# Performance work log

Hardware: AMD Instinct MI355X
Metric: run time of the kernel (lower is better)

## Reference

```python
import jax, jax.numpy as jnp
import numpy as np

# DCNv2 config (matches init_kwargs)
STRIDE, PAD, DIL = 1, 1, 1
KH, KW = 3, 3
K = KH * KW


def setup_inputs() -> dict:
    key = jax.random.key(0)
    k1, k2, k3, k4 = jax.random.split(key, 4)
    B, C, H, W = 2, 256, 96, 96
    O = 256
    inp = jax.random.normal(k1, (B, C, H, W), jnp.float32)
    # offset channels interleaved (dy, dx) per kernel tap -> 2*K channels
    offset = jax.random.normal(k2, (B, 2 * K, H, W), jnp.float32)
    # modulation mask in [0,1) (sigmoid is applied outside this module in DCN heads)
    mask = jax.random.uniform(k3, (B, K, H, W), jnp.float32)
    n = C * KH * KW
    stdv = 1.0 / float(np.sqrt(n))
    weight = jax.random.uniform(k4, (O, C, KH, KW), jnp.float32, -stdv, stdv)
    bias = jnp.zeros((O,), jnp.float32)
    return {"input": inp, "offset": offset, "mask": mask, "weight": weight, "bias": bias}


def reference(input, offset, mask, weight, bias):
    B, C, H, W = input.shape
    O = weight.shape[0]
    Ho = (H + 2 * PAD - DIL * (KH - 1) - 1) // STRIDE + 1
    Wo = (W + 2 * PAD - DIL * (KW - 1) - 1) // STRIDE + 1

    # learned per-pixel offsets: channel layout [dy_k0, dx_k0, dy_k1, dx_k1, ...]
    dy = offset[:, 0::2]  # [B,K,Ho,Wo]
    dx = offset[:, 1::2]  # [B,K,Ho,Wo]

    ky = (jnp.arange(K) // KW * DIL).astype(jnp.float32)  # kernel tap row offsets
    kx = (jnp.arange(K) % KW * DIL).astype(jnp.float32)   # kernel tap col offsets
    base_y = (jnp.arange(Ho) * STRIDE - PAD).astype(jnp.float32)
    base_x = (jnp.arange(Wo) * STRIDE - PAD).astype(jnp.float32)

    # sampling positions, [B,K,Ho,Wo]
    y = base_y[None, None, :, None] + ky[None, :, None, None] + dy
    x = base_x[None, None, None, :] + kx[None, :, None, None] + dx

    y0 = jnp.floor(y)
    x0 = jnp.floor(x)
    wy = y - y0  # bilinear fractional weights
    wx = x - x0

    inp_flat = input.reshape(B, C, H * W)

    def gather(yi, xi):
        # zero-padded bilinear corner gather: out-of-bounds -> 0
        ii = yi.astype(jnp.int32)
        jj = xi.astype(jnp.int32)
        valid = ((ii >= 0) & (ii < H) & (jj >= 0) & (jj < W)).astype(input.dtype)
        idx = jnp.clip(ii, 0, H - 1) * W + jnp.clip(jj, 0, W - 1)  # [B,K,Ho,Wo]
        v = jnp.take_along_axis(inp_flat, idx.reshape(B, 1, -1), axis=2)  # [B,C,K*Ho*Wo]
        return v * valid.reshape(B, 1, -1)

    v00 = gather(y0, x0)
    v01 = gather(y0, x0 + 1)
    v10 = gather(y0 + 1, x0)
    v11 = gather(y0 + 1, x0 + 1)

    wyf = wy.reshape(B, 1, -1)
    wxf = wx.reshape(B, 1, -1)
    sampled = (v00 * (1 - wyf) * (1 - wxf) + v01 * (1 - wyf) * wxf
               + v10 * wyf * (1 - wxf) + v11 * wyf * wxf)  # [B,C,K*Ho*Wo]

    mod = sampled * mask.reshape(B, 1, -1)           # modulation per tap/pixel
    mod = mod.reshape(B, C, K, Ho * Wo)
    out = jnp.einsum('bcks,ock->bos', mod, weight.reshape(O, C, K)) + bias[None, :, None]
    return out.reshape(B, O, Ho, Wo)
```

## Files before the change

### kernel.cpp

```cpp
#include <hip/hip_runtime.h>
#include <hip/hip_bf16.h>


#define Hh 96
#define Ww 96
#define Cc 256
#define Oo 256
#define Bb 2
#define Kk 9
#define Ss (Hh * Ww)
#define CKTOT (Cc * Kk)

typedef __bf16 bf16x8 __attribute__((ext_vector_type(8)));
typedef __bf16 bf16x2v __attribute__((ext_vector_type(2)));
typedef float f32x16 __attribute__((ext_vector_type(16)));
typedef float f32x2 __attribute__((ext_vector_type(2)));

__device__ __forceinline__ f32x2 up2(unsigned u) {
  f32x2 r;
  r.x = __uint_as_float(u << 16);
  r.y = __uint_as_float(u & 0xffff0000u);
  return r;
}

__device__ __forceinline__ void barrier_lgkm() {
  asm volatile("" ::: "memory");
  __builtin_amdgcn_s_waitcnt(0xC07F);
  __builtin_amdgcn_s_barrier();
  asm volatile("" ::: "memory");
}

__global__ __launch_bounds__(256) void prep(const float* __restrict__ inp,
                                            const float* __restrict__ wsrc,
                                            __bf16* __restrict__ it,
                                            __bf16* __restrict__ wt) {
  __shared__ float tile[64][65];
  const int bx = blockIdx.x;
  const int tid = threadIdx.x;

  if (bx < 1152) {
    const int hw0 = (bx % 144) * 64;
    const int c0 = ((bx / 144) & 3) * 64;
    const int b = bx / 576;
    const int hw_l = tid & 63, cr = tid >> 6;
    const float* src = inp + ((size_t)(b * Cc + c0) * Ss) + hw0;
#pragma unroll
    for (int r = 0; r < 16; ++r) {
      int c_l = r * 4 + cr;
      tile[c_l][hw_l] = src[(size_t)c_l * Ss + hw_l];
    }
    __syncthreads();
    const int cp = (tid & 31) * 2, hr = tid >> 5;
    __bf16* dst = it + ((size_t)(b * Ss + hw0) * Cc) + c0;
#pragma unroll
    for (int r = 0; r < 8; ++r) {
      int hw_s = r * 8 + hr;
      bf16x2v p;
      p.x = (__bf16)tile[cp][hw_s];
      p.y = (__bf16)tile[cp + 1][hw_s];
      *(bf16x2v*)(dst + (size_t)hw_s * Cc + cp) = p;
    }
  } else {
    int i = (bx - 1152) * 256 + tid;
    int j = i & 7;
    int l = (i >> 3) & 63;
    int cc = (i >> 9) & 15;
    int osub = (i >> 13) & 7;
    int kk = i >> 16;
    int o = osub * 32 + (l & 31);
    int ch = cc * 16 + ((l >> 5) << 3) + j;
    wt[i] = (__bf16)wsrc[(o * Cc + ch) * Kk + kk];
  }
}

__global__ __launch_bounds__(256, 4) void dcn_main(
    const __bf16* __restrict__ it,
    const __bf16* __restrict__ wt,
    const float* __restrict__ offset,
    const float* __restrict__ mask,
    const float* __restrict__ bias,
    float* __restrict__ out)
{
  __shared__ __bf16 colB[32 * 32 * 8];
  __shared__ int4 pa9[9][32];
  __shared__ float4 pw9[9][32];

  const int tid = threadIdx.x;
  const int tile = (blockIdx.x & 7) * 36 + (blockIdx.x >> 3);
  const int s0 = tile * 32;
  const int b = blockIdx.y;
  const int lane = tid & 63;
  const int wv = tid >> 6;
  const int sB = lane & 31;
  const int hi = lane >> 5;
  const int fs = tid & 31;
  const int gb = ((tid >> 5) & 1) + ((tid >> 6) << 1);

  const char* itb = (const char*)(it + (size_t)b * Ss * Cc);

  for (int idx = tid; idx < 9 * 32; idx += 256) {
    int kk = idx >> 5;
    int sl = idx & 31;
    int s = s0 + sl;
    int ho = s / Ww;
    int wo = s - ho * Ww;
    float dy = offset[((size_t)(b * 18 + 2 * kk)) * Ss + s];
    float dx = offset[((size_t)(b * 18 + 2 * kk + 1)) * Ss + s];
    float m = mask[((size_t)(b * 9 + kk)) * Ss + s];
    float y = (float)(ho - 1 + kk / 3) + dy;
    float x = (float)(wo - 1 + kk % 3) + dx;
    float fy = floorf(y), fx = floorf(x);
    int y0 = (int)fy, x0 = (int)fx;
    float wy = y - fy, wx = x - fx;
    int y1 = y0 + 1, x1 = x0 + 1;
    float vy0 = (y0 >= 0 && y0 < Hh) ? 1.f : 0.f;
    float vy1 = (y1 >= 0 && y1 < Hh) ? 1.f : 0.f;
    float vx0 = (x0 >= 0 && x0 < Ww) ? 1.f : 0.f;
    float vx1 = (x1 >= 0 && x1 < Ww) ? 1.f : 0.f;
    int y0c = min(max(y0, 0), Hh - 1), y1c = min(max(y1, 0), Hh - 1);
    int x0c = min(max(x0, 0), Ww - 1), x1c = min(max(x1, 0), Ww - 1);
    pa9[kk][sl] = make_int4((y0c * Ww + x0c) << 9, (y0c * Ww + x1c) << 9,
                            (y1c * Ww + x0c) << 9, (y1c * Ww + x1c) << 9);
    pw9[kk][sl] = make_float4(m * (1.f - wy) * (1.f - wx) * vy0 * vx0,
                              m * (1.f - wy) * wx * vy0 * vx1,
                              m * wy * (1.f - wx) * vy1 * vx0,
                              m * wy * wx * vy1 * vx1);
  }
  __syncthreads();

  f32x16 acc0, acc1;
#pragma unroll
  for (int j = 0; j < 16; ++j) { acc0[j] = 0.f; acc1[j] = 0.f; }

  for (int kk = 0; kk < Kk; ++kk) {
    if (kk) barrier_lgkm();

    const __bf16* pA = wt + (((size_t)(kk * 8 + wv * 2) * 16) << 9) + lane * 8;
    const __bf16* pB2 = pA + (16 << 9);
    bf16x8 WA0 = *(const bf16x8*)(pA);
    bf16x8 WB0 = *(const bf16x8*)(pB2);
    bf16x8 WA1 = *(const bf16x8*)(pA + 512);
    bf16x8 WB1 = *(const bf16x8*)(pB2 + 512);
    bf16x8 WA2 = *(const bf16x8*)(pA + 1024);
    bf16x8 WB2 = *(const bf16x8*)(pB2 + 1024);

    {
      int4 a = pa9[kk][fs];
      float4 wq = pw9[kk][fs];
#pragma unroll
      for (int half = 0; half < 2; ++half) {
        uint4 D[2][4];
#pragma unroll
        for (int q = 0; q < 2; ++q) {
          int g = gb + (half * 2 + q) * 8;
          const char* p = itb + g * 16;
          D[q][0] = *(const uint4*)(p + a.x);
          D[q][1] = *(const uint4*)(p + a.y);
          D[q][2] = *(const uint4*)(p + a.z);
          D[q][3] = *(const uint4*)(p + a.w);
        }
#pragma unroll
        for (int q = 0; q < 2; ++q) {
          int g = gb + (half * 2 + q) * 8;
          unsigned u0[4] = {D[q][0].x, D[q][0].y, D[q][0].z, D[q][0].w};
          unsigned u1[4] = {D[q][1].x, D[q][1].y, D[q][1].z, D[q][1].w};
          unsigned u2[4] = {D[q][2].x, D[q][2].y, D[q][2].z, D[q][2].w};
          unsigned u3[4] = {D[q][3].x, D[q][3].y, D[q][3].z, D[q][3].w};
          bf16x8 rv;
#pragma unroll
          for (int w = 0; w < 4; ++w) {
            f32x2 r = up2(u0[w]) * wq.x + up2(u1[w]) * wq.y +
                      up2(u2[w]) * wq.z + up2(u3[w]) * wq.w;
            rv[2 * w] = (__bf16)r.x;
            rv[2 * w + 1] = (__bf16)r.y;
          }
          *(bf16x8*)&colB[(g * 32 + fs) * 8] = rv;
        }
      }
    }
    barrier_lgkm();

    const __bf16* bp = &colB[(hi * 32 + sB) * 8];
    bf16x8 Bc = *(const bf16x8*)bp;
#pragma unroll
    for (int c = 0; c < 16; ++c) {
      bf16x8 Bn, WAn, WBn;
      if (c < 15) Bn = *(const bf16x8*)(bp + (c + 1) * 512);
      if (c < 13) {
        WAn = *(const bf16x8*)(pA + (c + 3) * 512);
        WBn = *(const bf16x8*)(pB2 + (c + 3) * 512);
      }
      acc0 = __builtin_amdgcn_mfma_f32_32x32x16_bf16(WA0, Bc, acc0, 0, 0, 0);
      acc1 = __builtin_amdgcn_mfma_f32_32x32x16_bf16(WB0, Bc, acc1, 0, 0, 0);
      WA0 = WA1; WB0 = WB1;
      WA1 = WA2; WB1 = WB2;
      if (c < 13) { WA2 = WAn; WB2 = WBn; }
      if (c < 15) Bc = Bn;
    }
  }

  float* ob = out + (size_t)b * Oo * Ss + s0 + sB;
#pragma unroll
  for (int os = 0; os < 2; ++os) {
#pragma unroll
    for (int r = 0; r < 16; ++r) {
      int o = wv * 64 + os * 32 + (r & 3) + 8 * (r >> 2) + 4 * hi;
      float v = (os ? acc1[r] : acc0[r]) + bias[o];
      ob[(size_t)o * Ss] = v;
    }
  }
}

extern "C" void kernel_launch(void* const* d_in, const int* in_sizes, int n_in,
                              void* d_out, int out_size, void* d_ws, size_t ws_size,
                              hipStream_t stream) {
  (void)in_sizes; (void)n_in; (void)out_size; (void)ws_size;
  const float* inp = (const float*)d_in[0];
  const float* offset = (const float*)d_in[1];
  const float* mask = (const float*)d_in[2];
  const float* weight = (const float*)d_in[3];
  const float* bias = (const float*)d_in[4];
  float* out = (float*)d_out;

  __bf16* it = (__bf16*)d_ws;
  __bf16* wt = (__bf16*)((char*)d_ws + (size_t)Bb * Ss * Cc * 2);

  prep<<<3456, 256, 0, stream>>>(inp, weight, it, wt);
  dcn_main<<<dim3(288, Bb), 256, 0, stream>>>(it, wt, offset, mask, bias, out);
}
```

Baseline: 157.7 us.

## Use 512-thread blocks with one output slab per wave and double-buffered swizzled colB

The block grows from 4 to 8 waves, and each wave now computes a single 32-output MFMA accumulator instead of two. This halves the per-wave MFMA and register work and doubles the waves available for the gather phase. The sampled column tile is double-buffered in LDS, which drops one barrier per tap, and an XOR swizzle is added to reduce bank conflicts. Weight fragments are prefetched deeper, eight registers ahead. The costs are more LDS per block, possible occupancy limits from the 512-thread launch bound, and more weight loads in total across waves.

```diff
diff --git a/kernel.cpp b/kernel.cpp
--- a/kernel.cpp
+++ b/kernel.cpp
@@ -73,7 +73,7 @@
   }
 }
 
-__global__ __launch_bounds__(256, 4) void dcn_main(
+__global__ __launch_bounds__(512, 4) void dcn_main(
     const __bf16* __restrict__ it,
     const __bf16* __restrict__ wt,
     const float* __restrict__ offset,
@@ -81,7 +81,7 @@
     const float* __restrict__ bias,
     float* __restrict__ out)
 {
-  __shared__ __bf16 colB[32 * 32 * 8];
+  __shared__ __bf16 colB[2][32 * 256];
   __shared__ int4 pa9[9][32];
   __shared__ float4 pw9[9][32];
 
@@ -90,17 +90,19 @@
   const int s0 = tile * 32;
   const int b = blockIdx.y;
   const int lane = tid & 63;
-  const int wv = tid >> 6;
+  const int w = tid >> 6;
   const int sB = lane & 31;
   const int hi = lane >> 5;
-  const int fs = tid & 31;
-  const int gb = ((tid >> 5) & 1) + ((tid >> 6) << 1);
+  const int pp = lane >> 4;
+  const int gq = lane & 15;
+  const int nf = w * 4 + pp;
+  const int swz = (nf ^ ((gq & 1) << 2));
 
   const char* itb = (const char*)(it + (size_t)b * Ss * Cc);
 
-  for (int idx = tid; idx < 9 * 32; idx += 256) {
-    int kk = idx >> 5;
-    int sl = idx & 31;
+  if (tid < 9 * 32) {
+    int kk = tid >> 5;
+    int sl = tid & 31;
     int s = s0 + sl;
     int ho = s / Ww;
     int wo = s - ho * Ww;
@@ -128,86 +130,69 @@
   }
   __syncthreads();
 
-  f32x16 acc0, acc1;
-#pragma unroll
-  for (int j = 0; j < 16; ++j) { acc0[j] = 0.f; acc1[j] = 0.f; }
+  f32x16 acc;
+#pragma unroll
+  for (int j = 0; j < 16; ++j) acc[j] = 0.f;
 
   for (int kk = 0; kk < Kk; ++kk) {
-    if (kk) barrier_lgkm();
-
-    const __bf16* pA = wt + (((size_t)(kk * 8 + wv * 2) * 16) << 9) + lane * 8;
-    const __bf16* pB2 = pA + (16 << 9);
-    bf16x8 WA0 = *(const bf16x8*)(pA);
-    bf16x8 WB0 = *(const bf16x8*)(pB2);
-    bf16x8 WA1 = *(const bf16x8*)(pA + 512);
-    bf16x8 WB1 = *(const bf16x8*)(pB2 + 512);
-    bf16x8 WA2 = *(const bf16x8*)(pA + 1024);
-    bf16x8 WB2 = *(const bf16x8*)(pB2 + 1024);
+    const int buf = kk & 1;
+    const __bf16* pW = wt + (((size_t)(kk * 8 + w) * 16) << 9) + (lane << 3);
+    bf16x8 Wr[8];
+#pragma unroll
+    for (int r = 0; r < 8; ++r) Wr[r] = *(const bf16x8*)(pW + r * 512);
 
     {
-      int4 a = pa9[kk][fs];
-      float4 wq = pw9[kk][fs];
-#pragma unroll
-      for (int half = 0; half < 2; ++half) {
-        uint4 D[2][4];
-#pragma unroll
-        for (int q = 0; q < 2; ++q) {
-          int g = gb + (half * 2 + q) * 8;
-          const char* p = itb + g * 16;
-          D[q][0] = *(const uint4*)(p + a.x);
-          D[q][1] = *(const uint4*)(p + a.y);
-          D[q][2] = *(const uint4*)(p + a.z);
-          D[q][3] = *(const uint4*)(p + a.w);
+      int4 a = pa9[kk][nf];
+      float4 wq = pw9[kk][nf];
+      uint4 D[2][4];
+#pragma unroll
+      for (int j = 0; j < 2; ++j) {
+        const char* p = itb + (j * 16 + gq) * 16;
+        D[j][0] = *(const uint4*)(p + a.x);
+        D[j][1] = *(const uint4*)(p + a.y);
+        D[j][2] = *(const uint4*)(p + a.z);
+        D[j][3] = *(const uint4*)(p + a.w);
+      }
+#pragma unroll
+      for (int j = 0; j < 2; ++j) {
+        unsigned u0[4] = {D[j][0].x, D[j][0].y, D[j][0].z, D[j][0].w};
+        unsigned u1[4] = {D[j][1].x, D[j][1].y, D[j][1].z, D[j][1].w};
+        unsigned u2[4] = {D[j][2].x, D[j][2].y, D[j][2].z, D[j][2].w};
+        unsigned u3[4] = {D[j][3].x, D[j][3].y, D[j][3].z, D[j][3].w};
+        bf16x8 rv;
+#pragma unroll
+        for (int d = 0; d < 4; ++d) {
+          f32x2 r = up2(u0[d]) * wq.x + up2(u1[d]) * wq.y +
+                    up2(u2[d]) * wq.z + up2(u3[d]) * wq.w;
+          rv[2 * d] = (__bf16)r.x;
+          rv[2 * d + 1] = (__bf16)r.y;
         }
-#pragma unroll
-        for (int q = 0; q < 2; ++q) {
-          int g = gb + (half * 2 + q) * 8;
-          unsigned u0[4] = {D[q][0].x, D[q][0].y, D[q][0].z, D[q][0].w};
-          unsigned u1[4] = {D[q][1].x, D[q][1].y, D[q][1].z, D[q][1].w};
-          unsigned u2[4] = {D[q][2].x, D[q][2].y, D[q][2].z, D[q][2].w};
-          unsigned u3[4] = {D[q][3].x, D[q][3].y, D[q][3].z, D[q][3].w};
-          bf16x8 rv;
-#pragma unroll
-          for (int w = 0; w < 4; ++w) {
-            f32x2 r = up2(u0[w]) * wq.x + up2(u1[w]) * wq.y +
-                      up2(u2[w]) * wq.z + up2(u3[w]) * wq.w;
-            rv[2 * w] = (__bf16)r.x;
-            rv[2 * w + 1] = (__bf16)r.y;
-          }
-          *(bf16x8*)&colB[(g * 32 + fs) * 8] = rv;
-        }
+        int g = j * 16 + gq;
+        *(bf16x8*)&colB[buf][g * 256 + swz * 8] = rv;
       }
     }
     barrier_lgkm();
 
-    const __bf16* bp = &colB[(hi * 32 + sB) * 8];
-    bf16x8 Bc = *(const bf16x8*)bp;
+    const __bf16* bp = &colB[buf][hi * 256 + ((sB ^ (hi << 2)) << 3)];
+    bf16x8 Br[4];
+#pragma unroll
+    for (int r = 0; r < 4; ++r) Br[r] = *(const bf16x8*)(bp + r * 512);
 #pragma unroll
     for (int c = 0; c < 16; ++c) {
-      bf16x8 Bn, WAn, WBn;
-      if (c < 15) Bn = *(const bf16x8*)(bp + (c + 1) * 512);
-      if (c < 13) {
-        WAn = *(const bf16x8*)(pA + (c + 3) * 512);
-        WBn = *(const bf16x8*)(pB2 + (c + 3) * 512);
-      }
-      acc0 = __builtin_amdgcn_mfma_f32_32x32x16_bf16(WA0, Bc, acc0, 0, 0, 0);
-      acc1 = __builtin_amdgcn_mfma_f32_32x32x16_bf16(WB0, Bc, acc1, 0, 0, 0);
-      WA0 = WA1; WB0 = WB1;
-      WA1 = WA2; WB1 = WB2;
-      if (c < 13) { WA2 = WAn; WB2 = WBn; }
-      if (c < 15) Bc = Bn;
+      bf16x8 Bn, Wn;
+      if (c < 12) Bn = *(const bf16x8*)(bp + (c + 4) * 512);
+      if (c < 8) Wn = *(const bf16x8*)(pW + (c + 8) * 512);
+      acc = __builtin_amdgcn_mfma_f32_32x32x16_bf16(Wr[c & 7], Br[c & 3], acc, 0, 0, 0);
+      if (c < 12) Br[c & 3] = Bn;
+      if (c < 8) Wr[c & 7] = Wn;
     }
   }
 
   float* ob = out + (size_t)b * Oo * Ss + s0 + sB;
 #pragma unroll
-  for (int os = 0; os < 2; ++os) {
-#pragma unroll
-    for (int r = 0; r < 16; ++r) {
-      int o = wv * 64 + os * 32 + (r & 3) + 8 * (r >> 2) + 4 * hi;
-      float v = (os ? acc1[r] : acc0[r]) + bias[o];
-      ob[(size_t)o * Ss] = v;
-    }
+  for (int r = 0; r < 16; ++r) {
+    int o = w * 32 + (r & 3) + 8 * (r >> 2) + 4 * hi;
+    ob[(size_t)o * Ss] = acc[r] + bias[o];
   }
 }
 
@@ -226,5 +211,5 @@
   __bf16* wt = (__bf16*)((char*)d_ws + (size_t)Bb * Ss * Cc * 2);
 
   prep<<<3456, 256, 0, stream>>>(inp, weight, it, wt);
-  dcn_main<<<dim3(288, Bb), 256, 0, stream>>>(it, wt, offset, mask, bias, out);
-}
+  dcn_main<<<dim3(288, Bb), 512, 0, stream>>>(it, wt, offset, mask, bias, out);
+}
```

Measured after the change: 131.1 us. 16.9% less time.
